# Kernel tuning notes

Measured on AMD Instinct MI355X. Metric: run time of the kernel, lower is better.

The kernel has to match this reference:

```python
import jax, jax.numpy as jnp
import numpy as np

D, H, S, L = 512, 8, 4, 2
HD = D // H          # 64 head dim
F = 4 * D            # 2048 FFN hidden
EPS = 1e-5


def setup_inputs() -> dict:
    key = jax.random.key(0)
    ks = jax.random.split(key, 26)
    B = 16384
    w = 0.02
    inp = {
        'text_pattern':   jax.random.normal(ks[0], (B, D), jnp.float32),
        'text_semantic':  jax.random.normal(ks[1], (B, D), jnp.float32),
        'image_pattern':  jax.random.normal(ks[2], (B, D), jnp.float32),
        'image_semantic': jax.random.normal(ks[3], (B, D), jnp.float32),
        # per-(layer, stream) attention projections, stacked [L,S,...]
        'Wq': jax.random.normal(ks[4], (L, S, D, D), jnp.float32) * w,
        'bq': jnp.zeros((L, S, D), jnp.float32),
        'Wk': jax.random.normal(ks[5], (L, S, D, D), jnp.float32) * w,
        'bk': jnp.zeros((L, S, D), jnp.float32),
        'Wv': jax.random.normal(ks[6], (L, S, D, D), jnp.float32) * w,
        'bv': jnp.zeros((L, S, D), jnp.float32),
        'Wo': jax.random.normal(ks[7], (L, S, D, D), jnp.float32) * w,
        'bo': jnp.zeros((L, S, D), jnp.float32),
        'ln_g': jnp.ones((L, S, D), jnp.float32),
        'ln_b': jnp.zeros((L, S, D), jnp.float32),
        'W1': jax.random.normal(ks[8], (L, S, D, F), jnp.float32) * w,
        'b1': jnp.zeros((L, S, F), jnp.float32),
        'W2': jax.random.normal(ks[9], (L, S, F, D), jnp.float32) * w,
        'b2': jnp.zeros((L, S, D), jnp.float32),
        # final fusion MLP: 4*D -> 2*D -> D
        'Wf1': jax.random.normal(ks[10], (S * D, 2 * D), jnp.float32) * w,
        'bf1': jnp.zeros((2 * D,), jnp.float32),
        'Wf2': jax.random.normal(ks[11], (2 * D, D), jnp.float32) * w,
        'bf2': jnp.zeros((D,), jnp.float32),
    }
    return inp


def _layer_norm(x, g, b):
    # x: [B,S,D], g/b: [S,D]; normalize over last dim
    mu = jnp.mean(x, axis=-1, keepdims=True)
    var = jnp.mean(jnp.square(x - mu), axis=-1, keepdims=True)
    return (x - mu) * jax.lax.rsqrt(var + EPS) * g + b


def reference(text_pattern, text_semantic, image_pattern, image_semantic,
              Wq, bq, Wk, bk, Wv, bv, Wo, bo, ln_g, ln_b,
              W1, b1, W2, b2, Wf1, bf1, Wf2, bf2):
    # streams stacked: [B, S=4, D]; each stream's query_len is 1, keys are all 4 streams
    x = jnp.stack([text_pattern, text_semantic, image_pattern, image_semantic], axis=1)
    B = x.shape[0]
    attn0 = None
    for l in range(L):
        # per-stream query projection of its own token: [B,S,D]
        q = jnp.einsum('bsd,sde->bse', x, Wq[l]) + bq[l]
        # per-stream K/V projections of ALL streams: [B,S(query-stream),K(key-pos),D]
        k = jnp.einsum('bkd,sde->bske', x, Wk[l]) + bk[l][:, None, :]
        v = jnp.einsum('bkd,sde->bske', x, Wv[l]) + bv[l][:, None, :]
        qh = q.reshape(B, S, H, HD)
        kh = k.reshape(B, S, S, H, HD)
        vh = v.reshape(B, S, S, H, HD)
        scores = jnp.einsum('bshe,bskhe->bshk', qh, kh) / (HD ** 0.5)  # [B,S,H,K]
        w = jax.nn.softmax(scores, axis=-1)
        ctx = jnp.einsum('bshk,bskhe->bshe', w, vh).reshape(B, S, D)
        attn_out = jnp.einsum('bsd,sde->bse', ctx, Wo[l]) + bo[l]
        if l == 0:
            attn0 = w  # [B,S,H,K]: layer-0 attention weights per stream
        h = _layer_norm(x + attn_out, ln_g[l], ln_b[l])
        ffn = jnp.einsum('bsf,sfd->bsd',
                         jax.nn.relu(jnp.einsum('bsd,sdf->bsf', h, W1[l]) + b1[l]),
                         W2[l]) + b2[l]
        x = h + ffn
    concat = x.reshape(B, S * D)
    fused = jax.nn.relu(concat @ Wf1 + bf1) @ Wf2 + bf2  # [B, D]
    return fused, attn0
```

## Files before the change

### kernel.cpp

```cpp
#include <hip/hip_runtime.h>
#include <stdint.h>

typedef unsigned short u16;
typedef __bf16 bf16x8 __attribute__((ext_vector_type(8)));
typedef float f32x4 __attribute__((ext_vector_type(4)));

constexpr int NB = 16384;
constexpr int DM = 512;
constexpr int NS = 4;
constexpr int FH = 2048;
constexpr int XW = NS * DM;
constexpr float EPSL = 1e-5f;

__device__ __forceinline__ float bf2f(u16 u) { return __uint_as_float(((uint32_t)u) << 16); }
__device__ __forceinline__ u16 f2bf(float f) {
  uint32_t u = __float_as_uint(f);
  u += 0x7fffu + ((u >> 16) & 1u);
  return (u16)(u >> 16);
}
__device__ __forceinline__ void unpack8(uint4 p, float* f) {
  f[0] = __uint_as_float(p.x << 16); f[1] = __uint_as_float(p.x & 0xffff0000u);
  f[2] = __uint_as_float(p.y << 16); f[3] = __uint_as_float(p.y & 0xffff0000u);
  f[4] = __uint_as_float(p.z << 16); f[5] = __uint_as_float(p.z & 0xffff0000u);
  f[6] = __uint_as_float(p.w << 16); f[7] = __uint_as_float(p.w & 0xffff0000u);
}
__device__ __forceinline__ uint4 pack8(const float* f) {
  uint4 r;
  r.x = (uint32_t)f2bf(f[0]) | ((uint32_t)f2bf(f[1]) << 16);
  r.y = (uint32_t)f2bf(f[2]) | ((uint32_t)f2bf(f[3]) << 16);
  r.z = (uint32_t)f2bf(f[4]) | ((uint32_t)f2bf(f[5]) << 16);
  r.w = (uint32_t)f2bf(f[6]) | ((uint32_t)f2bf(f[7]) << 16);
  return r;
}
__device__ __forceinline__ void gl_lds16(const void* g, void* l) {
  __builtin_amdgcn_global_load_lds((const __attribute__((address_space(1))) void*)g,
                                   (__attribute__((address_space(3))) void*)l, 16, 0, 0);
}

__device__ __forceinline__ void gemm_cv(
    const u16* __restrict__ A, int lda,
    const u16* __restrict__ Bt, int K,
    u16* As, u16* Bs, f32x4 (&acc)[4][4])
{
  const int tid = threadIdx.x;
  const int ln = tid & 63;
  const int w  = tid >> 6;
  const int wm = w >> 1, wn = w & 1;
  const int m0 = blockIdx.x * 128;
  const int n0 = blockIdx.y * 128;
  const int grow = ln >> 2;
  const int gcol = ((ln & 3) ^ ((ln >> 3) & 3)) * 8;
  const u16* Ab = A  + (size_t)(m0 + w * 32 + grow) * lda + gcol;
  const u16* Bb = Bt + (size_t)(n0 + w * 32 + grow) * K   + gcol;

  auto stage = [&](int buf, int k0) {
#pragma unroll
    for (int i = 0; i < 2; ++i) {
      gl_lds16(Ab + (size_t)i * 16 * lda + k0, &As[buf * 4096 + (w * 32 + i * 16) * 32]);
      gl_lds16(Bb + (size_t)i * 16 * K   + k0, &Bs[buf * 4096 + (w * 32 + i * 16) * 32]);
    }
  };

  __syncthreads();
  const int nt = K >> 5;
  stage(0, 0);
  if (nt > 1) {
    stage(1, 32);
    asm volatile("s_waitcnt vmcnt(4)" ::: "memory");
  } else {
    asm volatile("s_waitcnt vmcnt(0)" ::: "memory");
  }
  __builtin_amdgcn_s_barrier();
  asm volatile("" ::: "memory");

  const int rx = ((ln & 15) >> 1) & 3;
  const int qb = ln >> 4;
  const int cb = (qb ^ rx) * 8;
  int cur = 0, nxt2 = 2;
  for (int t = 0; t < nt; ++t) {
    bf16x8 af[4], bfv[4];
#pragma unroll
    for (int m = 0; m < 4; ++m) {
      af[m]  = *(const bf16x8*)&As[cur * 4096 + (wm * 64 + m * 16 + (ln & 15)) * 32 + cb];
      bfv[m] = *(const bf16x8*)&Bs[cur * 4096 + (wn * 64 + m * 16 + (ln & 15)) * 32 + cb];
    }
#pragma unroll
    for (int m = 0; m < 4; ++m)
#pragma unroll
      for (int n = 0; n < 4; ++n)
        acc[m][n] = __builtin_amdgcn_mfma_f32_16x16x32_bf16(af[m], bfv[n], acc[m][n], 0, 0, 0);
    if (t + 2 < nt) {
      stage(nxt2, (t + 2) * 32);
      asm volatile("s_waitcnt vmcnt(4)" ::: "memory");
      __builtin_amdgcn_s_barrier();
      asm volatile("" ::: "memory");
    } else if (t + 1 < nt) {
      asm volatile("s_waitcnt vmcnt(0)" ::: "memory");
      __builtin_amdgcn_s_barrier();
      asm volatile("" ::: "memory");
    }
    cur = cur + 1;  if (cur == 3)  cur = 0;
    nxt2 = nxt2 + 1; if (nxt2 == 3) nxt2 = 0;
  }
  asm volatile("" ::: "memory");
}

template<bool RELU, bool RESID, bool OUTF32>
__global__ __launch_bounds__(256) void k_gemm(
    const u16* __restrict__ A, int lda, long aZ,
    const u16* __restrict__ Bt, long bZ,
    const float* __restrict__ bias, long biasZ,
    const u16* __restrict__ Rsd, int ldr, long rZ,
    void* __restrict__ Cp, int ldc, long cZ, int K)
{
  const int z = blockIdx.z;
  A += (long)z * aZ; Bt += (long)z * bZ; bias += (long)z * biasZ;
  __shared__ alignas(16) u16 As[3 * 4096];
  __shared__ alignas(16) u16 Bs[3 * 4096];
  f32x4 acc[4][4] = {};
  gemm_cv(A, lda, Bt, K, As, Bs, acc);
  const int ln = threadIdx.x & 63;
  const int w = threadIdx.x >> 6;
  const int wm = w >> 1, wn = w & 1;
  const int m0 = blockIdx.x * 128, n0 = blockIdx.y * 128;
#pragma unroll
  for (int n = 0; n < 4; ++n) {
    const int gc = n0 + wn * 64 + n * 16 + (ln & 15);
    const float bv = bias[gc];
#pragma unroll
    for (int m = 0; m < 4; ++m) {
#pragma unroll
      for (int j = 0; j < 4; ++j) {
        const int gr = m0 + wm * 64 + m * 16 + (ln >> 4) * 4 + j;
        float v = acc[m][n][j] + bv;
        if constexpr (RESID) v += bf2f(Rsd[(long)z * rZ + (size_t)gr * ldr + gc]);
        if constexpr (RELU)  v = v > 0.f ? v : 0.f;
        if constexpr (OUTF32) ((float*)Cp)[(long)z * cZ + (size_t)gr * ldc + gc] = v;
        else                  ((u16*)Cp)[(long)z * cZ + (size_t)gr * ldc + gc] = f2bf(v);
      }
    }
  }
}

__global__ __launch_bounds__(256) void k_kdot(
    const u16* __restrict__ xcat, const u16* __restrict__ WkT_l,
    const u16* __restrict__ Qb, float* __restrict__ wbuf)
{
  const int s = blockIdx.z >> 2, kp = blockIdx.z & 3;
  __shared__ alignas(16) u16 As[3 * 4096];
  __shared__ alignas(16) u16 Bs[3 * 4096];
  f32x4 acc[4][4] = {};
  gemm_cv(xcat + kp * DM, XW, WkT_l + (size_t)s * DM * DM, DM, As, Bs, acc);
  const int ln = threadIdx.x & 63;
  const int w = threadIdx.x >> 6;
  const int wm = w >> 1, wn = w & 1;
  const int m0 = blockIdx.x * 128, n0 = blockIdx.y * 128;
  const int h = (n0 >> 6) + wn;
  float p[4][4];
#pragma unroll
  for (int m = 0; m < 4; ++m)
#pragma unroll
    for (int j = 0; j < 4; ++j) p[m][j] = 0.f;
#pragma unroll
  for (int n = 0; n < 4; ++n) {
    const int gc = n0 + wn * 64 + n * 16 + (ln & 15);
#pragma unroll
    for (int m = 0; m < 4; ++m) {
#pragma unroll
      for (int j = 0; j < 4; ++j) {
        const int gr = m0 + wm * 64 + m * 16 + (ln >> 4) * 4 + j;
        p[m][j] += acc[m][n][j] * bf2f(Qb[((size_t)s * NB + gr) * DM + gc]);
      }
    }
  }
#pragma unroll
  for (int m = 0; m < 4; ++m)
#pragma unroll
    for (int j = 0; j < 4; ++j) {
      float v = p[m][j];
      v += __shfl_xor(v, 1, 64);
      v += __shfl_xor(v, 2, 64);
      v += __shfl_xor(v, 4, 64);
      v += __shfl_xor(v, 8, 64);
      p[m][j] = v;
    }
  if ((ln & 15) == 0) {
#pragma unroll
    for (int m = 0; m < 4; ++m)
#pragma unroll
      for (int j = 0; j < 4; ++j) {
        const int gr = m0 + wm * 64 + m * 16 + (ln >> 4) * 4 + j;
        wbuf[(((size_t)s * NB + gr) * 8 + h) * 4 + kp] = p[m][j] * 0.125f;
      }
  }
}

__global__ __launch_bounds__(256) void k_gemmv4(
    const u16* __restrict__ xcat, const u16* __restrict__ WvT_l,
    const float* __restrict__ bv_l, const float* __restrict__ wbuf,
    u16* __restrict__ ctxc)
{
  __shared__ alignas(16) u16 As[3 * 4096];
  __shared__ alignas(16) u16 Bs[3 * 4096];
  const int ln = threadIdx.x & 63;
  const int w = threadIdx.x >> 6;
  const int wm = w >> 1, wn = w & 1;
  const int m0 = blockIdx.x * 128, n0 = blockIdx.y * 128;
  const int s  = n0 >> 9;
  const int hh = ((n0 >> 6) + wn) & 7;
  f32x4 facc[4][4] = {};
  for (int kp = 0; kp < 4; ++kp) {
    f32x4 acc[4][4] = {};
    gemm_cv(xcat + kp * DM, XW, WvT_l, DM, As, Bs, acc);
    float wv[4][4];
#pragma unroll
    for (int m = 0; m < 4; ++m)
#pragma unroll
      for (int j = 0; j < 4; ++j) {
        const int gr = m0 + wm * 64 + m * 16 + (ln >> 4) * 4 + j;
        wv[m][j] = wbuf[(((size_t)s * NB + gr) * 8 + hh) * 4 + kp];
      }
#pragma unroll
    for (int n = 0; n < 4; ++n) {
      const float bvv = bv_l[n0 + wn * 64 + n * 16 + (ln & 15)];
#pragma unroll
      for (int m = 0; m < 4; ++m)
#pragma unroll
        for (int j = 0; j < 4; ++j)
          facc[m][n][j] += (acc[m][n][j] + bvv) * wv[m][j];
    }
  }
#pragma unroll
  for (int n = 0; n < 4; ++n) {
    const int gc = n0 + wn * 64 + n * 16 + (ln & 15);
#pragma unroll
    for (int m = 0; m < 4; ++m)
#pragma unroll
      for (int j = 0; j < 4; ++j) {
        const int gr = m0 + wm * 64 + m * 16 + (ln >> 4) * 4 + j;
        ctxc[(size_t)gr * XW + gc] = f2bf(facc[m][n][j]);
      }
  }
}

__global__ __launch_bounds__(256) void k_softmax(
    float* __restrict__ wbuf, float* __restrict__ a0)
{
  const int t = blockIdx.x * 256 + threadIdx.x;
  float4 v = ((const float4*)wbuf)[t];
  const float mx = fmaxf(fmaxf(v.x, v.y), fmaxf(v.z, v.w));
  float4 e;
  e.x = __expf(v.x - mx); e.y = __expf(v.y - mx);
  e.z = __expf(v.z - mx); e.w = __expf(v.w - mx);
  const float inv = 1.f / (e.x + e.y + e.z + e.w);
  e.x *= inv; e.y *= inv; e.z *= inv; e.w *= inv;
  ((float4*)wbuf)[t] = e;
  if (a0 != nullptr) {
    const int s = t >> 17, b = (t >> 3) & (NB - 1), h = t & 7;
    ((float4*)a0)[((size_t)b * NS + s) * 8 + h] = e;
  }
}

__global__ __launch_bounds__(256) void k_ln(
    u16* __restrict__ xcat, const float* __restrict__ g, const float* __restrict__ bb)
{
  const int ln = threadIdx.x & 63;
  const int row = blockIdx.x * 4 + (threadIdx.x >> 6);
  const int b = row >> 2, s = row & 3;
  u16* p = xcat + (size_t)b * XW + s * DM;
  float v[8];
  { uint4 t = ((const uint4*)p)[ln]; unpack8(t, v); }
  float sum = 0.f;
#pragma unroll
  for (int j = 0; j < 8; ++j) sum += v[j];
#pragma unroll
  for (int off = 1; off < 64; off <<= 1) sum += __shfl_xor(sum, off, 64);
  const float mu = sum * (1.f / DM);
  float s2 = 0.f;
#pragma unroll
  for (int j = 0; j < 8; ++j) { float d = v[j] - mu; s2 += d * d; }
#pragma unroll
  for (int off = 1; off < 64; off <<= 1) s2 += __shfl_xor(s2, off, 64);
  const float rs = rsqrtf(s2 * (1.f / DM) + EPSL);
  const int e0 = s * DM + ln * 8;
  float o[8];
#pragma unroll
  for (int j = 0; j < 8; ++j) o[j] = (v[j] - mu) * rs * g[e0 + j] + bb[e0 + j];
  ((uint4*)p)[ln] = pack8(o);
}

__global__ void k_pack(const float* __restrict__ t0, const float* __restrict__ t1,
                       const float* __restrict__ t2, const float* __restrict__ t3,
                       u16* __restrict__ xcat)
{
  const int total = NB * XW / 8;
  for (int t = blockIdx.x * blockDim.x + threadIdx.x; t < total; t += gridDim.x * blockDim.x) {
    const int b = t >> 8;
    const int r = t & 255;
    const int s = r >> 6;
    const int d0 = (r & 63) * 8;
    const float* p = (s == 0) ? t0 : (s == 1) ? t1 : (s == 2) ? t2 : t3;
    float f[8];
#pragma unroll
    for (int j = 0; j < 8; ++j) f[j] = p[(size_t)b * DM + d0 + j];
    ((uint4*)xcat)[t] = pack8(f);
  }
}

__global__ void k_tcvt(const float* __restrict__ src, u16* __restrict__ dst,
                       int rlog, int clog, int nb)
{
  const int mlog = rlog + clog;
  const size_t total = (size_t)nb << mlog;
  for (size_t t = (size_t)blockIdx.x * blockDim.x + threadIdx.x; t < total;
       t += (size_t)gridDim.x * blockDim.x) {
    const size_t mat = t >> mlog;
    const uint32_t rem = (uint32_t)(t & ((1u << mlog) - 1));
    const uint32_t n = rem >> rlog;
    const uint32_t r = rem & ((1u << rlog) - 1);
    dst[t] = f2bf(src[(mat << mlog) + ((size_t)r << clog) + n]);
  }
}

extern "C" void kernel_launch(void* const* d_in, const int* in_sizes, int n_in,
                              void* d_out, int out_size, void* d_ws, size_t ws_size,
                              hipStream_t stream)
{
  (void)in_sizes; (void)n_in; (void)out_size;
  const float* t0  = (const float*)d_in[0];
  const float* t1  = (const float*)d_in[1];
  const float* t2  = (const float*)d_in[2];
  const float* t3  = (const float*)d_in[3];
  const float* Wq  = (const float*)d_in[4];
  const float* bq  = (const float*)d_in[5];
  const float* Wk  = (const float*)d_in[6];
  const float* Wv  = (const float*)d_in[8];
  const float* bv  = (const float*)d_in[9];
  const float* Wo  = (const float*)d_in[10];
  const float* bo  = (const float*)d_in[11];
  const float* lng = (const float*)d_in[12];
  const float* lnb = (const float*)d_in[13];
  const float* W1  = (const float*)d_in[14];
  const float* b1  = (const float*)d_in[15];
  const float* W2  = (const float*)d_in[16];
  const float* b2  = (const float*)d_in[17];
  const float* Wf1 = (const float*)d_in[18];
  const float* bf1 = (const float*)d_in[19];
  const float* Wf2 = (const float*)d_in[20];
  const float* bf2 = (const float*)d_in[21];

  size_t off = 0;
  char* ws = (char*)d_ws;
  auto take = [&](size_t n) { char* p = ws + off; off += (n + 255) & ~(size_t)255; return p; };
  u16* WqT  = (u16*)take(8ull * DM * DM * 2);
  u16* WkT  = (u16*)take(8ull * DM * DM * 2);
  u16* WvT  = (u16*)take(8ull * DM * DM * 2);
  u16* WoT  = (u16*)take(8ull * DM * DM * 2);
  u16* W1T  = (u16*)take(8ull * DM * FH * 2);
  u16* W2T  = (u16*)take(8ull * FH * DM * 2);
  u16* Wf1T = (u16*)take((size_t)XW * 1024 * 2);
  u16* Wf2T = (u16*)take((size_t)1024 * DM * 2);
  u16* xcat = (u16*)take((size_t)NB * XW * 2);
  char* U1  = take((size_t)NB * XW * 2);
  float* wbuf = (float*)take(4ull * NB * 8 * 4 * 4);
  const size_t needed = off;

  u16* Qb   = (u16*)U1;
  u16* ctxc = (u16*)U1;
  u16* ffn1 = (u16*)U1;
  u16* y1   = (u16*)U1;
  float* attn0 = (float*)d_out + (size_t)NB * DM;

  if (needed > ws_size) return;

  k_tcvt<<<dim3(1024), dim3(256), 0, stream>>>(Wq, WqT, 9, 9, 8);
  k_tcvt<<<dim3(1024), dim3(256), 0, stream>>>(Wk, WkT, 9, 9, 8);
  k_tcvt<<<dim3(1024), dim3(256), 0, stream>>>(Wv, WvT, 9, 9, 8);
  k_tcvt<<<dim3(1024), dim3(256), 0, stream>>>(Wo, WoT, 9, 9, 8);
  k_tcvt<<<dim3(1024), dim3(256), 0, stream>>>(W1, W1T, 9, 11, 8);
  k_tcvt<<<dim3(1024), dim3(256), 0, stream>>>(W2, W2T, 11, 9, 8);
  k_tcvt<<<dim3(1024), dim3(256), 0, stream>>>(Wf1, Wf1T, 11, 10, 1);
  k_tcvt<<<dim3(1024), dim3(256), 0, stream>>>(Wf2, Wf2T, 10, 9, 1);
  k_pack<<<dim3(2048), dim3(256), 0, stream>>>(t0, t1, t2, t3, xcat);

  const size_t WSQ = (size_t)DM * DM;
  for (int ly = 0; ly < 2; ++ly) {
    const u16* WqT_l = WqT + (size_t)ly * 4 * WSQ;
    const u16* WkT_l = WkT + (size_t)ly * 4 * WSQ;
    const u16* WvT_l = WvT + (size_t)ly * 4 * WSQ;
    const u16* WoT_l = WoT + (size_t)ly * 4 * WSQ;
    k_gemm<false, false, false><<<dim3(128, 4, 4), dim3(256), 0, stream>>>(
        xcat, XW, DM, WqT_l, WSQ, bq + (size_t)ly * XW, DM,
        nullptr, 0, 0, Qb, DM, (long)NB * DM, DM);
    k_kdot<<<dim3(128, 4, 16), dim3(256), 0, stream>>>(xcat, WkT_l, Qb, wbuf);
    k_softmax<<<dim3(4 * NB * 8 / 256), dim3(256), 0, stream>>>(
        wbuf, (ly == 0) ? attn0 : (float*)nullptr);
    k_gemmv4<<<dim3(128, 16), dim3(256), 0, stream>>>(
        xcat, WvT_l, bv + (size_t)ly * XW, wbuf, ctxc);
    k_gemm<false, true, false><<<dim3(128, 4, 4), dim3(256), 0, stream>>>(
        ctxc, XW, DM, WoT_l, WSQ, bo + (size_t)ly * XW, DM,
        xcat, XW, DM, xcat, XW, DM, DM);
    k_ln<<<dim3(NB), dim3(256), 0, stream>>>(xcat, lng + ly * XW, lnb + ly * XW);
    for (int s = 0; s < NS; ++s) {
      const size_t wsl = (size_t)(ly * 4 + s);
      k_gemm<true, false, false><<<dim3(128, 16, 1), dim3(256), 0, stream>>>(
          xcat + s * DM, XW, 0, W1T + wsl * (size_t)DM * FH, 0, b1 + wsl * FH, 0,
          nullptr, 0, 0, ffn1, FH, 0, DM);
      k_gemm<false, true, false><<<dim3(128, 4, 1), dim3(256), 0, stream>>>(
          ffn1, FH, 0, W2T + wsl * (size_t)FH * DM, 0, b2 + wsl * DM, 0,
          xcat + s * DM, XW, 0, xcat + s * DM, XW, 0, FH);
    }
  }
  k_gemm<true, false, false><<<dim3(128, 8, 1), dim3(256), 0, stream>>>(
      xcat, XW, 0, Wf1T, 0, bf1, 0, nullptr, 0, 0, y1, 1024, 0, XW);
  k_gemm<false, false, true><<<dim3(128, 4, 1), dim3(256), 0, stream>>>(
      y1, 1024, 0, Wf2T, 0, bf2, 0, nullptr, 0, 0, d_out, DM, 0, 1024);
}
```

Before: 2.700 ms.

## Chain multiple GEMM segments per block with continuous pipelining and XCD-aware remap

Replaces the per-tile GEMM core with a segment-chained loop, so one block runs several consecutive GEMMs (streams, key positions or row chunks) and keeps the triple-buffered LDS prefetch going across segment boundaries, running an epilogue at the end of each segment. Grids shrink (for example, the z-dimension for Q/O and the kdot grid are folded into the chain), and block IDs are remapped so contiguous M tiles land on the same XCD, which should improve L2 reuse of shared operands. The aim is to remove pipeline warm-up and drain bubbles and to reduce launch and tail costs. The trade-off is fewer blocks in flight for some GEMMs, which may lower occupancy and load balance, and the remap assumes gridDim.x is divisible by 8.

New measurement: 4.078 ms. +51.0%, slower.

```diff
diff --git a/kernel.cpp b/kernel.cpp
--- a/kernel.cpp
+++ b/kernel.cpp
@@ -37,47 +37,57 @@
                                    (__attribute__((address_space(3))) void*)l, 16, 0, 0);
 }
 
-__device__ __forceinline__ void gemm_cv(
-    const u16* __restrict__ A, int lda,
-    const u16* __restrict__ Bt, int K,
-    u16* As, u16* Bs, f32x4 (&acc)[4][4])
+__device__ __forceinline__ void remap(int& bx, int& by, int& bz) {
+  const int gx = gridDim.x, gy = gridDim.y;
+  const int fl = (blockIdx.z * gy + blockIdx.y) * gx + blockIdx.x;
+  const int xcd = fl & 7;
+  const int t = fl >> 3;
+  const int bw = gx >> 3;
+  bx = xcd * bw + t % bw;
+  const int u = t / bw;
+  by = u % gy;
+  bz = u / gy;
+}
+
+template<int NSEG, class Epi>
+__device__ __forceinline__ void gemm_chain(
+    const u16* __restrict__ A, long segA, int lda,
+    const u16* __restrict__ Bt, long segB, int K, int ntl,
+    u16* As, u16* Bs, int m0, int n0, Epi epi)
 {
   const int tid = threadIdx.x;
   const int ln = tid & 63;
   const int w  = tid >> 6;
   const int wm = w >> 1, wn = w & 1;
-  const int m0 = blockIdx.x * 128;
-  const int n0 = blockIdx.y * 128;
   const int grow = ln >> 2;
   const int gcol = ((ln & 3) ^ ((ln >> 3) & 3)) * 8;
   const u16* Ab = A  + (size_t)(m0 + w * 32 + grow) * lda + gcol;
   const u16* Bb = Bt + (size_t)(n0 + w * 32 + grow) * K   + gcol;
-
-  auto stage = [&](int buf, int k0) {
+  const int nt = K >> 5, NT = nt * NSEG, ntm = nt - 1;
+
+  auto stage = [&](int buf, int v) {
+    const int seg = v >> ntl;
+    const int k0 = (v & ntm) << 5;
+    const u16* a = Ab + (long)seg * segA + k0;
+    const u16* b = Bb + (long)seg * segB + k0;
 #pragma unroll
     for (int i = 0; i < 2; ++i) {
-      gl_lds16(Ab + (size_t)i * 16 * lda + k0, &As[buf * 4096 + (w * 32 + i * 16) * 32]);
-      gl_lds16(Bb + (size_t)i * 16 * K   + k0, &Bs[buf * 4096 + (w * 32 + i * 16) * 32]);
+      gl_lds16(a + (size_t)(i * 16) * lda, &As[buf * 4096 + (w * 32 + i * 16) * 32]);
+      gl_lds16(b + (size_t)(i * 16) * K,   &Bs[buf * 4096 + (w * 32 + i * 16) * 32]);
     }
   };
 
-  __syncthreads();
-  const int nt = K >> 5;
+  f32x4 acc[4][4] = {};
   stage(0, 0);
-  if (nt > 1) {
-    stage(1, 32);
-    asm volatile("s_waitcnt vmcnt(4)" ::: "memory");
-  } else {
-    asm volatile("s_waitcnt vmcnt(0)" ::: "memory");
-  }
+  stage(1, 1);
+  asm volatile("s_waitcnt vmcnt(4)" ::: "memory");
   __builtin_amdgcn_s_barrier();
   asm volatile("" ::: "memory");
 
-  const int rx = ((ln & 15) >> 1) & 3;
-  const int qb = ln >> 4;
-  const int cb = (qb ^ rx) * 8;
-  int cur = 0, nxt2 = 2;
-  for (int t = 0; t < nt; ++t) {
+  const int cb = ((ln >> 4) ^ (((ln & 15) >> 1) & 3)) * 8;
+  int cur = 0, nxt = 2;
+  for (int v = 0; v < NT; ++v) {
+    if (v + 2 < NT) stage(nxt, v + 2);
     bf16x8 af[4], bfv[4];
 #pragma unroll
     for (int m = 0; m < 4; ++m) {
@@ -89,129 +99,132 @@
 #pragma unroll
       for (int n = 0; n < 4; ++n)
         acc[m][n] = __builtin_amdgcn_mfma_f32_16x16x32_bf16(af[m], bfv[n], acc[m][n], 0, 0, 0);
-    if (t + 2 < nt) {
-      stage(nxt2, (t + 2) * 32);
-      asm volatile("s_waitcnt vmcnt(4)" ::: "memory");
-      __builtin_amdgcn_s_barrier();
-      asm volatile("" ::: "memory");
-    } else if (t + 1 < nt) {
-      asm volatile("s_waitcnt vmcnt(0)" ::: "memory");
-      __builtin_amdgcn_s_barrier();
-      asm volatile("" ::: "memory");
-    }
-    cur = cur + 1;  if (cur == 3)  cur = 0;
-    nxt2 = nxt2 + 1; if (nxt2 == 3) nxt2 = 0;
-  }
-  asm volatile("" ::: "memory");
-}
-
-template<bool RELU, bool RESID, bool OUTF32>
+    if ((v & ntm) == ntm) {
+      epi(v >> ntl, acc);
+#pragma unroll
+      for (int m = 0; m < 4; ++m)
+#pragma unroll
+        for (int n = 0; n < 4; ++n) acc[m][n] = f32x4{0.f, 0.f, 0.f, 0.f};
+    }
+    if (v + 2 < NT)      asm volatile("s_waitcnt vmcnt(4)" ::: "memory");
+    else if (v + 1 < NT) asm volatile("s_waitcnt vmcnt(0)" ::: "memory");
+    else break;
+    __builtin_amdgcn_s_barrier();
+    asm volatile("" ::: "memory");
+    cur = cur + 1; if (cur == 3) cur = 0;
+    nxt = nxt + 1; if (nxt == 3) nxt = 0;
+  }
+}
+
+template<bool RELU, bool RESID, bool OUTF32, int NSEG>
 __global__ __launch_bounds__(256) void k_gemm(
-    const u16* __restrict__ A, int lda, long aZ,
-    const u16* __restrict__ Bt, long bZ,
+    const u16* __restrict__ A, long segA, int lda, int mspan, int segM,
+    const u16* __restrict__ Bt, long segB,
     const float* __restrict__ bias, long biasZ,
     const u16* __restrict__ Rsd, int ldr, long rZ,
-    void* __restrict__ Cp, int ldc, long cZ, int K)
-{
-  const int z = blockIdx.z;
-  A += (long)z * aZ; Bt += (long)z * bZ; bias += (long)z * biasZ;
-  __shared__ alignas(16) u16 As[3 * 4096];
-  __shared__ alignas(16) u16 Bs[3 * 4096];
-  f32x4 acc[4][4] = {};
-  gemm_cv(A, lda, Bt, K, As, Bs, acc);
-  const int ln = threadIdx.x & 63;
-  const int w = threadIdx.x >> 6;
-  const int wm = w >> 1, wn = w & 1;
-  const int m0 = blockIdx.x * 128, n0 = blockIdx.y * 128;
-#pragma unroll
-  for (int n = 0; n < 4; ++n) {
-    const int gc = n0 + wn * 64 + n * 16 + (ln & 15);
-    const float bv = bias[gc];
-#pragma unroll
-    for (int m = 0; m < 4; ++m) {
-#pragma unroll
-      for (int j = 0; j < 4; ++j) {
-        const int gr = m0 + wm * 64 + m * 16 + (ln >> 4) * 4 + j;
-        float v = acc[m][n][j] + bv;
-        if constexpr (RESID) v += bf2f(Rsd[(long)z * rZ + (size_t)gr * ldr + gc]);
-        if constexpr (RELU)  v = v > 0.f ? v : 0.f;
-        if constexpr (OUTF32) ((float*)Cp)[(long)z * cZ + (size_t)gr * ldc + gc] = v;
-        else                  ((u16*)Cp)[(long)z * cZ + (size_t)gr * ldc + gc] = f2bf(v);
-      }
-    }
-  }
-}
-
-__global__ __launch_bounds__(256) void k_kdot(
-    const u16* __restrict__ xcat, const u16* __restrict__ WkT_l,
-    const u16* __restrict__ Qb, float* __restrict__ wbuf)
-{
-  const int s = blockIdx.z >> 2, kp = blockIdx.z & 3;
-  __shared__ alignas(16) u16 As[3 * 4096];
-  __shared__ alignas(16) u16 Bs[3 * 4096];
-  f32x4 acc[4][4] = {};
-  gemm_cv(xcat + kp * DM, XW, WkT_l + (size_t)s * DM * DM, DM, As, Bs, acc);
-  const int ln = threadIdx.x & 63;
-  const int w = threadIdx.x >> 6;
-  const int wm = w >> 1, wn = w & 1;
-  const int m0 = blockIdx.x * 128, n0 = blockIdx.y * 128;
-  const int h = (n0 >> 6) + wn;
-  float p[4][4];
-#pragma unroll
-  for (int m = 0; m < 4; ++m)
-#pragma unroll
-    for (int j = 0; j < 4; ++j) p[m][j] = 0.f;
-#pragma unroll
-  for (int n = 0; n < 4; ++n) {
-    const int gc = n0 + wn * 64 + n * 16 + (ln & 15);
-#pragma unroll
-    for (int m = 0; m < 4; ++m) {
-#pragma unroll
-      for (int j = 0; j < 4; ++j) {
-        const int gr = m0 + wm * 64 + m * 16 + (ln >> 4) * 4 + j;
-        p[m][j] += acc[m][n][j] * bf2f(Qb[((size_t)s * NB + gr) * DM + gc]);
-      }
-    }
-  }
-#pragma unroll
-  for (int m = 0; m < 4; ++m)
-#pragma unroll
-    for (int j = 0; j < 4; ++j) {
-      float v = p[m][j];
-      v += __shfl_xor(v, 1, 64);
-      v += __shfl_xor(v, 2, 64);
-      v += __shfl_xor(v, 4, 64);
-      v += __shfl_xor(v, 8, 64);
-      p[m][j] = v;
-    }
-  if ((ln & 15) == 0) {
-#pragma unroll
-    for (int m = 0; m < 4; ++m)
-#pragma unroll
-      for (int j = 0; j < 4; ++j) {
-        const int gr = m0 + wm * 64 + m * 16 + (ln >> 4) * 4 + j;
-        wbuf[(((size_t)s * NB + gr) * 8 + h) * 4 + kp] = p[m][j] * 0.125f;
-      }
-  }
-}
-
-__global__ __launch_bounds__(256) void k_gemmv4(
-    const u16* __restrict__ xcat, const u16* __restrict__ WvT_l,
-    const float* __restrict__ bv_l, const float* __restrict__ wbuf,
-    u16* __restrict__ ctxc)
-{
+    void* __restrict__ Cp, int ldc, long cZ, int K, int ntl)
+{
+  int bx, by, bz; remap(bx, by, bz); (void)bz;
   __shared__ alignas(16) u16 As[3 * 4096];
   __shared__ alignas(16) u16 Bs[3 * 4096];
   const int ln = threadIdx.x & 63;
   const int w = threadIdx.x >> 6;
   const int wm = w >> 1, wn = w & 1;
-  const int m0 = blockIdx.x * 128, n0 = blockIdx.y * 128;
+  const int m0 = bx * mspan, n0 = by * 128;
+  auto epi = [&](int seg, f32x4 (&acc)[4][4]) {
+    const float* bs = bias + (long)seg * biasZ;
+#pragma unroll
+    for (int n = 0; n < 4; ++n) {
+      const int gc = n0 + wn * 64 + n * 16 + (ln & 15);
+      const float bv = bs[gc];
+#pragma unroll
+      for (int m = 0; m < 4; ++m) {
+#pragma unroll
+        for (int j = 0; j < 4; ++j) {
+          const int gr = m0 + seg * segM + wm * 64 + m * 16 + (ln >> 4) * 4 + j;
+          float v = acc[m][n][j] + bv;
+          if constexpr (RESID) v += bf2f(Rsd[(long)seg * rZ + (size_t)gr * ldr + gc]);
+          if constexpr (RELU)  v = v > 0.f ? v : 0.f;
+          if constexpr (OUTF32) ((float*)Cp)[(long)seg * cZ + (size_t)gr * ldc + gc] = v;
+          else                  ((u16*)Cp)[(long)seg * cZ + (size_t)gr * ldc + gc] = f2bf(v);
+        }
+      }
+    }
+  };
+  gemm_chain<NSEG>(A, segA, lda, Bt, segB, K, ntl, As, Bs, m0, n0, epi);
+}
+
+__global__ __launch_bounds__(256) void k_kdot(
+    const u16* __restrict__ xcat, const u16* __restrict__ WkT_l,
+    const u16* __restrict__ Qb, float* __restrict__ wbuf)
+{
+  int bx, by, s; remap(bx, by, s);
+  __shared__ alignas(16) u16 As[3 * 4096];
+  __shared__ alignas(16) u16 Bs[3 * 4096];
+  const int ln = threadIdx.x & 63;
+  const int w = threadIdx.x >> 6;
+  const int wm = w >> 1, wn = w & 1;
+  const int m0 = bx * 128, n0 = by * 128;
+  const int h = (n0 >> 6) + wn;
+  auto epi = [&](int kp, f32x4 (&acc)[4][4]) {
+    float p[4][4];
+#pragma unroll
+    for (int m = 0; m < 4; ++m)
+#pragma unroll
+      for (int j = 0; j < 4; ++j) p[m][j] = 0.f;
+#pragma unroll
+    for (int n = 0; n < 4; ++n) {
+      const int gc = n0 + wn * 64 + n * 16 + (ln & 15);
+#pragma unroll
+      for (int m = 0; m < 4; ++m) {
+#pragma unroll
+        for (int j = 0; j < 4; ++j) {
+          const int gr = m0 + wm * 64 + m * 16 + (ln >> 4) * 4 + j;
+          p[m][j] += acc[m][n][j] * bf2f(Qb[((size_t)s * NB + gr) * DM + gc]);
+        }
+      }
+    }
+#pragma unroll
+    for (int m = 0; m < 4; ++m)
+#pragma unroll
+      for (int j = 0; j < 4; ++j) {
+        float v = p[m][j];
+        v += __shfl_xor(v, 1, 64);
+        v += __shfl_xor(v, 2, 64);
+        v += __shfl_xor(v, 4, 64);
+        v += __shfl_xor(v, 8, 64);
+        p[m][j] = v;
+      }
+    if ((ln & 15) == 0) {
+#pragma unroll
+      for (int m = 0; m < 4; ++m)
+#pragma unroll
+        for (int j = 0; j < 4; ++j) {
+          const int gr = m0 + wm * 64 + m * 16 + (ln >> 4) * 4 + j;
+          wbuf[(((size_t)s * NB + gr) * 8 + h) * 4 + kp] = p[m][j] * 0.125f;
+        }
+    }
+  };
+  gemm_chain<4>(xcat, DM, XW, WkT_l + (size_t)s * DM * DM, 0, DM, 4,
+                As, Bs, m0, n0, epi);
+}
+
+__global__ __launch_bounds__(256) void k_gemmv4(
+    const u16* __restrict__ xcat, const u16* __restrict__ WvT_l,
+    const float* __restrict__ bv_l, const float* __restrict__ wbuf,
+    u16* __restrict__ ctxc)
+{
+  int bx, by, bz; remap(bx, by, bz); (void)bz;
+  __shared__ alignas(16) u16 As[3 * 4096];
+  __shared__ alignas(16) u16 Bs[3 * 4096];
+  const int ln = threadIdx.x & 63;
+  const int w = threadIdx.x >> 6;
+  const int wm = w >> 1, wn = w & 1;
+  const int m0 = bx * 128, n0 = by * 128;
   const int s  = n0 >> 9;
   const int hh = ((n0 >> 6) + wn) & 7;
   f32x4 facc[4][4] = {};
-  for (int kp = 0; kp < 4; ++kp) {
-    f32x4 acc[4][4] = {};
-    gemm_cv(xcat + kp * DM, XW, WvT_l, DM, As, Bs, acc);
+  auto epi = [&](int kp, f32x4 (&acc)[4][4]) {
     float wv[4][4];
 #pragma unroll
     for (int m = 0; m < 4; ++m)
@@ -229,7 +242,8 @@
         for (int j = 0; j < 4; ++j)
           facc[m][n][j] += (acc[m][n][j] + bvv) * wv[m][j];
     }
-  }
+  };
+  gemm_chain<4>(xcat, DM, XW, WvT_l, 0, DM, 4, As, Bs, m0, n0, epi);
 #pragma unroll
   for (int n = 0; n < 4; ++n) {
     const int gc = n0 + wn * 64 + n * 16 + (ln & 15);
@@ -383,36 +397,37 @@
   k_tcvt<<<dim3(1024), dim3(256), 0, stream>>>(Wf2, Wf2T, 10, 9, 1);
   k_pack<<<dim3(2048), dim3(256), 0, stream>>>(t0, t1, t2, t3, xcat);
 
-  const size_t WSQ = (size_t)DM * DM;
+  const long WSQ = (long)DM * DM;
   for (int ly = 0; ly < 2; ++ly) {
     const u16* WqT_l = WqT + (size_t)ly * 4 * WSQ;
     const u16* WkT_l = WkT + (size_t)ly * 4 * WSQ;
     const u16* WvT_l = WvT + (size_t)ly * 4 * WSQ;
     const u16* WoT_l = WoT + (size_t)ly * 4 * WSQ;
-    k_gemm<false, false, false><<<dim3(128, 4, 4), dim3(256), 0, stream>>>(
-        xcat, XW, DM, WqT_l, WSQ, bq + (size_t)ly * XW, DM,
-        nullptr, 0, 0, Qb, DM, (long)NB * DM, DM);
-    k_kdot<<<dim3(128, 4, 16), dim3(256), 0, stream>>>(xcat, WkT_l, Qb, wbuf);
+    k_gemm<false, false, false, 4><<<dim3(128, 4), dim3(256), 0, stream>>>(
+        xcat, DM, XW, 128, 0, WqT_l, WSQ, bq + (size_t)ly * XW, DM,
+        nullptr, 0, 0, Qb, DM, (long)NB * DM, DM, 4);
+    k_kdot<<<dim3(128, 4, 4), dim3(256), 0, stream>>>(xcat, WkT_l, Qb, wbuf);
     k_softmax<<<dim3(4 * NB * 8 / 256), dim3(256), 0, stream>>>(
         wbuf, (ly == 0) ? attn0 : (float*)nullptr);
     k_gemmv4<<<dim3(128, 16), dim3(256), 0, stream>>>(
         xcat, WvT_l, bv + (size_t)ly * XW, wbuf, ctxc);
-    k_gemm<false, true, false><<<dim3(128, 4, 4), dim3(256), 0, stream>>>(
-        ctxc, XW, DM, WoT_l, WSQ, bo + (size_t)ly * XW, DM,
-        xcat, XW, DM, xcat, XW, DM, DM);
+    k_gemm<false, true, false, 4><<<dim3(128, 4), dim3(256), 0, stream>>>(
+        ctxc, DM, XW, 128, 0, WoT_l, WSQ, bo + (size_t)ly * XW, DM,
+        xcat, XW, DM, xcat, XW, DM, DM, 4);
     k_ln<<<dim3(NB), dim3(256), 0, stream>>>(xcat, lng + ly * XW, lnb + ly * XW);
     for (int s = 0; s < NS; ++s) {
       const size_t wsl = (size_t)(ly * 4 + s);
-      k_gemm<true, false, false><<<dim3(128, 16, 1), dim3(256), 0, stream>>>(
-          xcat + s * DM, XW, 0, W1T + wsl * (size_t)DM * FH, 0, b1 + wsl * FH, 0,
-          nullptr, 0, 0, ffn1, FH, 0, DM);
-      k_gemm<false, true, false><<<dim3(128, 4, 1), dim3(256), 0, stream>>>(
-          ffn1, FH, 0, W2T + wsl * (size_t)FH * DM, 0, b2 + wsl * DM, 0,
-          xcat + s * DM, XW, 0, xcat + s * DM, XW, 0, FH);
-    }
-  }
-  k_gemm<true, false, false><<<dim3(128, 8, 1), dim3(256), 0, stream>>>(
-      xcat, XW, 0, Wf1T, 0, bf1, 0, nullptr, 0, 0, y1, 1024, 0, XW);
-  k_gemm<false, false, true><<<dim3(128, 4, 1), dim3(256), 0, stream>>>(
-      y1, 1024, 0, Wf2T, 0, bf2, 0, nullptr, 0, 0, d_out, DM, 0, 1024);
-}
+      k_gemm<true, false, false, 4><<<dim3(32, 16), dim3(256), 0, stream>>>(
+          xcat + s * DM, (long)128 * XW, XW, 512, 128,
+          W1T + wsl * (size_t)DM * FH, 0, b1 + wsl * FH, 0,
+          nullptr, 0, 0, ffn1, FH, 0, DM, 4);
+      k_gemm<false, true, false, 1><<<dim3(128, 4), dim3(256), 0, stream>>>(
+          ffn1, 0, FH, 128, 0, W2T + wsl * (size_t)FH * DM, 0, b2 + wsl * DM, 0,
+          xcat + s * DM, XW, 0, xcat + s * DM, XW, 0, FH, 6);
+    }
+  }
+  k_gemm<true, false, false, 1><<<dim3(128, 8), dim3(256), 0, stream>>>(
+      xcat, 0, XW, 128, 0, Wf1T, 0, bf1, 0, nullptr, 0, 0, y1, 1024, 0, XW, 6);
+  k_gemm<false, false, true, 1><<<dim3(128, 4), dim3(256), 0, stream>>>(
+      y1, 0, 1024, 128, 0, Wf2T, 0, bf2, 0, nullptr, 0, 0, d_out, DM, 0, 1024, 5);
+}
```
